# Performance work log

Hardware: AMD Instinct MI355X
Metric: run time of the kernel (lower is better)

Reference implementation:

```python
import jax, jax.numpy as jnp
import numpy as np
from jax.ops import segment_sum

N_NODES = 500000
N_EDGES = 1000000
N_GRAPHS = 20000
F_IN = 78


def gcn_conv(x, W, b, src, dst, n):
    # PyG GCNConv: add self-loops, symmetric normalization D^-1/2 A D^-1/2
    h = x @ W  # [N, Fout]
    deg = segment_sum(jnp.ones(src.shape[0], x.dtype), dst, num_segments=n) + 1.0  # self-loop
    dinv = jax.lax.rsqrt(deg)  # [N]
    norm = dinv[src] * dinv[dst]  # [E]
    agg = segment_sum(h[src] * norm[:, None], dst, num_segments=n)  # neighbor messages
    agg = agg + h * (dinv * dinv)[:, None]  # self-loop message
    return agg + b


def global_mean_pool(x, batch, n_graphs):
    s = segment_sum(x, batch, num_segments=n_graphs)
    cnt = segment_sum(jnp.ones(x.shape[0], x.dtype), batch, num_segments=n_graphs)
    return s / jnp.maximum(cnt, 1.0)[:, None]


def setup_inputs() -> dict:
    key = jax.random.key(0)
    ks = jax.random.split(key, 16)
    x = jax.random.normal(ks[0], (N_NODES, F_IN), dtype=jnp.float32)
    edge_index = jax.random.randint(ks[1], (2, N_EDGES), 0, N_NODES, dtype=jnp.int32)
    batch = jnp.sort(jax.random.randint(ks[2], (N_NODES,), 0, N_GRAPHS, dtype=jnp.int32))

    def lin(k, fi, fo):
        s = 1.0 / np.sqrt(fi)
        kw, kb = jax.random.split(k)
        return (jax.random.uniform(kw, (fi, fo), jnp.float32, -s, s),
                jax.random.uniform(kb, (fo,), jnp.float32, -s, s))

    W1, b1 = lin(ks[3], F_IN, F_IN)
    W2, b2 = lin(ks[4], F_IN, F_IN * 2)
    W3, b3 = lin(ks[5], F_IN * 2, F_IN * 4)
    fW1, fb1 = lin(ks[6], F_IN * 4, 1024)
    fW2, fb2 = lin(ks[7], 1024, 128)
    return {"x": x, "edge_index": edge_index, "batch": batch,
            "W1": W1, "b1": b1, "W2": W2, "b2": b2, "W3": W3, "b3": b3,
            "fW1": fW1, "fb1": fb1, "fW2": fW2, "fb2": fb2}


def reference(x, edge_index, batch, W1, b1, W2, b2, W3, b3, fW1, fb1, fW2, fb2):
    src, dst = edge_index[0], edge_index[1]
    n = x.shape[0]
    h = jax.nn.relu(gcn_conv(x, W1, b1, src, dst, n))
    h = jax.nn.relu(gcn_conv(h, W2, b2, src, dst, n))
    h = jax.nn.relu(gcn_conv(h, W3, b3, src, dst, n))
    g = global_mean_pool(h, batch, N_GRAPHS)  # [G, 312]
    g = jax.nn.relu(g @ fW1 + fb1)  # dropout is identity at eval
    return g @ fW2 + fb2
```

## Files before the change

kernel.cpp:

```cpp
#include <hip/hip_runtime.h>
#include <hip/hip_fp16.h>

#define N_NODES 500000
#define N_EDGES 1000000
#define N_GRAPHS 20000

typedef _Float16 f16x8 __attribute__((ext_vector_type(8)));
typedef float f32x4 __attribute__((ext_vector_type(4)));

__global__ __launch_bounds__(256) void fill_u32(unsigned* p, unsigned v, int n) {
  int i = blockIdx.x * 256 + threadIdx.x;
  if (i < n) p[i] = v;
}

__global__ __launch_bounds__(256) void hist_dst(const int* __restrict__ dst, int* cnt, int e) {
  int i = blockIdx.x * 256 + threadIdx.x;
  if (i < e) atomicAdd(&cnt[dst[i]], 1);
}

__global__ __launch_bounds__(256) void scanA(const int* __restrict__ deg, int* __restrict__ loc,
                                             int* __restrict__ partials, int n) {
  __shared__ int ts[256];
  int b = blockIdx.x, t = threadIdx.x;
  int base = b * 1024 + t * 4;
  int v[4], s = 0;
#pragma unroll
  for (int j = 0; j < 4; ++j) {
    v[j] = (base + j < n) ? deg[base + j] : 0;
    s += v[j];
  }
  ts[t] = s;
  __syncthreads();
  for (int off = 1; off < 256; off <<= 1) {
    int x = (t >= off) ? ts[t - off] : 0;
    __syncthreads();
    ts[t] += x;
    __syncthreads();
  }
  if (t == 255) partials[b] = ts[255];
  int run = ts[t] - s;
#pragma unroll
  for (int j = 0; j < 4; ++j) {
    if (base + j < n) loc[base + j] = run;
    run += v[j];
  }
}

__global__ __launch_bounds__(512) void scanB(int* partials, int nb) {
  __shared__ int s[512];
  int t = threadIdx.x;
  s[t] = (t < nb) ? partials[t] : 0;
  __syncthreads();
  if (t == 0) {
    int run = 0;
    for (int i = 0; i < nb; ++i) { int v = s[i]; s[i] = run; run += v; }
  }
  __syncthreads();
  if (t < nb) partials[t] = s[t];
}

__global__ __launch_bounds__(256) void scanC(int* __restrict__ rowptr, const int* __restrict__ partials,
                                             int* __restrict__ cur, int n, int e) {
  int i = blockIdx.x * 256 + threadIdx.x;
  if (i < n) {
    int v = rowptr[i] + partials[i >> 10];
    rowptr[i] = v;
    cur[i] = v;
  }
  if (i == 0) rowptr[n] = e;
}

__global__ __launch_bounds__(256) void dinv_k(const int* __restrict__ rowptr, float* dinv, int n) {
  int i = blockIdx.x * 256 + threadIdx.x;
  if (i < n) dinv[i] = rsqrtf(1.0f + (float)(rowptr[i + 1] - rowptr[i]));
}

__global__ __launch_bounds__(256) void bucket(const int* __restrict__ src, const int* __restrict__ dst,
                                              int* __restrict__ cur, int* __restrict__ ssrc, int e) {
  int i = blockIdx.x * 256 + threadIdx.x;
  if (i < e) ssrc[atomicAdd(&cur[dst[i]], 1)] = src[i];
}

__global__ __launch_bounds__(256) void ell_build(const int* __restrict__ rowptr,
                                                 const int* __restrict__ ssrc,
                                                 int4* __restrict__ ell, int n) {
  int i = blockIdx.x * 256 + threadIdx.x;
  if (i >= n) return;
  int r0 = rowptr[i], r1 = rowptr[i + 1];
  int deg = r1 - r0;
  int4 e;
  e.x = deg;
  e.y = (deg > 0) ? ssrc[r0] : 0;
  e.z = (deg > 1) ? ssrc[r0 + 1] : 0;
  e.w = (deg > 2) ? ssrc[r0 + 2] : 0;
  ell[i] = e;
}

__global__ __launch_bounds__(256) void graph_starts(const int* __restrict__ batch,
                                                    int* __restrict__ gstart, int n) {
  int i = blockIdx.x * 256 + threadIdx.x;
  if (i < n) {
    int b = batch[i];
    int bp = (i == 0) ? -1 : batch[i - 1];
    for (int g = bp + 1; g <= b; ++g) gstart[g] = i;
  } else if (i == n) {
    int bl = batch[n - 1];
    for (int g = bl + 1; g <= N_GRAPHS; ++g) gstart[g] = n;
  }
}

template <int CW>
__global__ __launch_bounds__(256) void wt_conv(const float* __restrict__ W, _Float16* __restrict__ WT,
                                               int K, int Nout, int ldw, int KPL, int STRIDE, int total) {
  int i = blockIdx.x * 256 + threadIdx.x;
  if (i >= total) return;
  int c = i / STRIDE, kp = i - c * STRIDE;
  int k = kp; bool valid = kp < KPL;
  if (CW) { int blk = kp / CW, r = kp - blk * CW; k = blk * 78 + r; valid = valid && (r < 78) && (k < K); }
  else { valid = valid && (kp < K); }
  WT[i] = (valid && c < Nout) ? (_Float16)W[(size_t)k * ldw + c] : (_Float16)0.f;
}

__global__ __launch_bounds__(256) void xconv(const float* __restrict__ xin,
                                             const float* __restrict__ dinv,
                                             _Float16* __restrict__ Xh) {
  unsigned idx = blockIdx.x * 256u + threadIdx.x;
  if (idx >= (unsigned)N_NODES * 52u) return;
  unsigned n = idx / 52u, c2 = idx - n * 52u;
  __half2 h = __floats2half2_rn(0.f, 0.f);
  if (c2 < 39u) {
    float di = dinv[n];
    float2 v = *reinterpret_cast<const float2*>(xin + (size_t)n * 78 + 2 * c2);
    h = __floats2half2_rn(v.x * di, v.y * di);
  }
  *reinterpret_cast<__half2*>((__half*)Xh + (size_t)n * 104 + 2 * c2) = h;
}

__device__ __forceinline__ void async16(const void* g, void* l) {
  __builtin_amdgcn_global_load_lds(
      (const __attribute__((address_space(1))) void*)g,
      (__attribute__((address_space(3))) void*)l, 16, 0, 0);
}

template <int KPL, int STRIDE, int OUT_MODE>
__global__ __launch_bounds__(256) void gemm_lds(
    const _Float16* __restrict__ in, const _Float16* __restrict__ WT,
    _Float16* __restrict__ outp, const float* __restrict__ rs,
    const float* __restrict__ bo, int M, int LDO) {
  constexpr int NS = KPL / 32;
  constexpr int SB = STRIDE * 2;
  constexpr int CA = (64 * SB) / 1024;
  constexpr int CB = (80 * SB + 1023) / 1024;
  __shared__ __align__(16) _Float16 As[64 * STRIDE];
  __shared__ __align__(16) _Float16 Bs[CB * 512];
  const int tid = threadIdx.x;
  const int lane = tid & 63;
  const int wid = tid >> 6;
  const int row0 = blockIdx.y * 64;
  const _Float16* wt = WT + (size_t)(blockIdx.x * 78) * STRIDE;
  _Float16* out = outp + (size_t)blockIdx.x * 80;
  const float* bop = bo + blockIdx.x * 78;

  const char* ab = (const char*)in + (size_t)row0 * SB;
  for (int c = wid; c < CA; c += 4)
    async16(ab + (size_t)c * 1024 + lane * 16, (char*)As + c * 1024);
  const char* bb = (const char*)wt;
  for (int c = wid; c < CB; c += 4)
    async16(bb + (size_t)c * 1024 + lane * 16, (char*)Bs + c * 1024);
  __syncthreads();

  const int r16 = lane & 15, q = lane >> 4;
  const f32x4 z4 = {0.f, 0.f, 0.f, 0.f};
  f32x4 acc[5];
#pragma unroll
  for (int nf = 0; nf < 5; ++nf) acc[nf] = z4;

#pragma unroll
  for (int s = 0; s < NS; ++s) {
    f16x8 af = *reinterpret_cast<const f16x8*>(&As[(wid * 16 + r16) * STRIDE + s * 32 + q * 8]);
#pragma unroll
    for (int nf = 0; nf < 5; ++nf) {
      f16x8 bf = *reinterpret_cast<const f16x8*>(&Bs[(nf * 16 + r16) * STRIDE + s * 32 + q * 8]);
      acc[nf] = __builtin_amdgcn_mfma_f32_16x16x32_f16(af, bf, acc[nf], 0, 0, 0);
    }
  }

  __syncthreads();
  _Float16* Os = As;
#pragma unroll
  for (int j = 0; j < 4; ++j) {
    int rl = wid * 16 + q * 4 + j;
    int gr = row0 + rl;
    float sc = (OUT_MODE == 3 && gr < M) ? rs[gr] : 1.f;
#pragma unroll
    for (int nf = 0; nf < 5; ++nf) {
      int cl = nf * 16 + r16;
      float v = 0.f;
      if (cl < 78) {
        v = fmaxf(acc[nf][j] + bop[cl], 0.f);
        if (OUT_MODE == 3) v *= sc;
      }
      Os[rl * 80 + cl] = (_Float16)v;
    }
  }
  __syncthreads();
  for (int i = tid; i < 640; i += 256) {
    int rl = i / 10, u = i - rl * 10;
    int gr = row0 + rl;
    if (gr < M)
      *reinterpret_cast<uint4*>(&out[(size_t)gr * LDO + u * 8]) =
          *reinterpret_cast<const uint4*>(&Os[rl * 80 + u * 8]);
  }
}

template <int KP, int OUT_MODE, int BLDS>
__global__ __launch_bounds__(256) void gemm_direct(
    const _Float16* __restrict__ in, const _Float16* __restrict__ WT,
    void* __restrict__ outp, const float* __restrict__ bo,
    int M, int Nout, int LDO) {
  constexpr int NS = KP / 32;
  constexpr bool TSTORE = (BLDS != 0) && (OUT_MODE != 2);
  constexpr int BS_BYTES = BLDS ? 5 * NS * 64 * 16 : 16;
  constexpr int SM_BYTES = TSTORE ? (BS_BYTES > 20480 ? BS_BYTES : 20480) : BS_BYTES;
  __shared__ __align__(16) char smem[SM_BYTES];
  _Float16* Bs = (_Float16*)smem;
  const int tid = threadIdx.x;
  const int lane = tid & 63;
  const int wid = tid >> 6;
  const int row0 = blockIdx.y * 128;
  const int col0 = blockIdx.x * 80;
  const _Float16* wt = WT + (size_t)col0 * KP;
  _Float16* out16 = (_Float16*)outp;
  float* out32 = (float*)outp;
  const int koff = (lane >> 4) * 8;
  const int gr0 = row0 + wid * 32 + (lane & 15);
  const bool v0 = gr0 < M, v1 = (gr0 + 16) < M;
  const _Float16* a0 = in + (size_t)gr0 * KP + koff;
  const _Float16* a1 = a0 + (size_t)16 * KP;
  const _Float16* bp = wt + (size_t)(lane & 15) * KP + koff;

  if (BLDS) {
    for (int i = tid; i < 5 * NS * 64; i += 256) {
      int l = i & 63;
      int nf = (i >> 6) % 5;
      int s = i / 320;
      int r = nf * 16 + (l & 15);
      int k = s * 32 + ((l >> 4) << 3);
      *reinterpret_cast<uint4*>(&Bs[(size_t)i * 8]) =
          *reinterpret_cast<const uint4*>(wt + (size_t)r * KP + k);
    }
    __syncthreads();
  }

  const f16x8 zf = {0, 0, 0, 0, 0, 0, 0, 0};
  const f32x4 z4 = {0.f, 0.f, 0.f, 0.f};
  f32x4 acc[2][5];
#pragma unroll
  for (int a = 0; a < 2; ++a)
#pragma unroll
    for (int b = 0; b < 5; ++b) acc[a][b] = z4;

#pragma unroll
  for (int s = 0; s < NS; ++s) {
    f16x8 af0 = v0 ? *reinterpret_cast<const f16x8*>(a0 + s * 32) : zf;
    f16x8 af1 = v1 ? *reinterpret_cast<const f16x8*>(a1 + s * 32) : zf;
    f16x8 bf[5];
#pragma unroll
    for (int nf = 0; nf < 5; ++nf) {
      if (BLDS)
        bf[nf] = *reinterpret_cast<const f16x8*>(&Bs[((size_t)(s * 5 + nf) * 64 + lane) * 8]);
      else
        bf[nf] = *reinterpret_cast<const f16x8*>(bp + (size_t)nf * 16 * KP + s * 32);
    }
#pragma unroll
    for (int nf = 0; nf < 5; ++nf) {
      acc[0][nf] = __builtin_amdgcn_mfma_f32_16x16x32_f16(af0, bf[nf], acc[0][nf], 0, 0, 0);
      acc[1][nf] = __builtin_amdgcn_mfma_f32_16x16x32_f16(af1, bf[nf], acc[1][nf], 0, 0, 0);
    }
  }

  if constexpr (TSTORE) {
    __syncthreads();
    _Float16* Os = (_Float16*)smem;
#pragma unroll
    for (int rf = 0; rf < 2; ++rf) {
#pragma unroll
      for (int j = 0; j < 4; ++j) {
        int rl = wid * 32 + rf * 16 + (lane >> 4) * 4 + j;
#pragma unroll
        for (int nf = 0; nf < 5; ++nf) {
          int cl = nf * 16 + (lane & 15);
          int oc = col0 + cl;
          float r = 0.f;
          if (oc < Nout) r = fmaxf(acc[rf][nf][j] + bo[oc], 0.f);
          Os[rl * 80 + cl] = (_Float16)r;
        }
      }
    }
    __syncthreads();
    for (int i = tid; i < 1280; i += 256) {
      int rl = i / 10, u = i - rl * 10;
      int gr = row0 + rl;
      if (gr < M)
        *reinterpret_cast<uint4*>(&out16[(size_t)gr * LDO + col0 + u * 8]) =
            *reinterpret_cast<const uint4*>(&Os[rl * 80 + u * 8]);
    }
  } else {
#pragma unroll
    for (int rf = 0; rf < 2; ++rf) {
#pragma unroll
      for (int j = 0; j < 4; ++j) {
        int gr = row0 + wid * 32 + rf * 16 + (lane >> 4) * 4 + j;
        if (gr >= M) continue;
#pragma unroll
        for (int nf = 0; nf < 5; ++nf) {
          int oc = col0 + nf * 16 + (lane & 15);
          if (oc >= Nout) continue;
          float v = acc[rf][nf][j];
          if (OUT_MODE == 1) out16[(size_t)gr * LDO + oc] = (_Float16)fmaxf(v + bo[oc], 0.f);
          else out32[(size_t)gr * LDO + oc] = v + bo[oc];
        }
      }
    }
  }
}

__device__ inline void acc8(float* a, uint4 v) {
  const __half2* h = reinterpret_cast<const __half2*>(&v);
#pragma unroll
  for (int j = 0; j < 4; ++j) {
    float2 f = __half22float2(h[j]);
    a[2 * j] += f.x;
    a[2 * j + 1] += f.y;
  }
}

template <int LDI>
__device__ inline void gather_sumT(float* a, const _Float16* hbase, unsigned n,
                                   const int4* __restrict__ ell,
                                   const int* __restrict__ rowptr,
                                   const int* __restrict__ ssrc) {
  int4 e = ell[n];
  const int deg = e.x;
  uint4 sv = *reinterpret_cast<const uint4*>(hbase + (size_t)n * LDI);
  uint4 g0, g1, g2;
  if (deg > 0) g0 = *reinterpret_cast<const uint4*>(hbase + (size_t)e.y * LDI);
  if (deg > 1) g1 = *reinterpret_cast<const uint4*>(hbase + (size_t)e.z * LDI);
  if (deg > 2) g2 = *reinterpret_cast<const uint4*>(hbase + (size_t)e.w * LDI);
  {
    const __half2* h = reinterpret_cast<const __half2*>(&sv);
#pragma unroll
    for (int j = 0; j < 4; ++j) {
      float2 f = __half22float2(h[j]);
      a[2 * j] = f.x;
      a[2 * j + 1] = f.y;
    }
  }
  if (deg > 0) acc8(a, g0);
  if (deg > 1) acc8(a, g1);
  if (deg > 2) acc8(a, g2);
  if (deg > 3) {
    int r = rowptr[n] + 3, r1 = r + deg - 3;
    for (; r + 2 <= r1; r += 2) {
      uint4 va = *reinterpret_cast<const uint4*>(hbase + (size_t)ssrc[r] * LDI);
      uint4 vb = *reinterpret_cast<const uint4*>(hbase + (size_t)ssrc[r + 1] * LDI);
      acc8(a, va);
      acc8(a, vb);
    }
    if (r < r1) {
      uint4 va = *reinterpret_cast<const uint4*>(hbase + (size_t)ssrc[r] * LDI);
      acc8(a, va);
    }
  }
}

template <int LDI, int NSUB>
__global__ __launch_bounds__(256) void aggregateZ(
    const _Float16* __restrict__ in, const int4* __restrict__ ell,
    const int* __restrict__ rowptr, const int* __restrict__ ssrc,
    const float* __restrict__ dinv, _Float16* __restrict__ outZ, int ldo) {
  unsigned idx = blockIdx.x * 256u + threadIdx.x;
  if (idx >= (unsigned)N_NODES * NSUB) return;
  unsigned n = idx / NSUB, sub = idx - n * NSUB;
  float a[8];
  gather_sumT<LDI>(a, in + sub * 8u, n, ell, rowptr, ssrc);
  float di = dinv[n];
  _Float16 ov[8];
#pragma unroll
  for (int j = 0; j < 8; ++j) ov[j] = (_Float16)(di * a[j]);
  *reinterpret_cast<uint4*>(outZ + (size_t)n * ldo + sub * 8u) =
      *reinterpret_cast<const uint4*>(ov);
}

__global__ __launch_bounds__(256) void pool_seq(
    const _Float16* __restrict__ in, const int* __restrict__ gstart,
    _Float16* __restrict__ GA, int inOff, int coffGA) {
  unsigned idx = blockIdx.x * 256u + threadIdx.x;
  if (idx >= (unsigned)N_GRAPHS * 10u) return;
  unsigned g = idx / 10u, q = idx - g * 10u;
  int n0 = gstart[g], n1 = gstart[g + 1];
  const _Float16* base = in + inOff + q * 8;
  float a[8] = {0.f, 0.f, 0.f, 0.f, 0.f, 0.f, 0.f, 0.f};
  float b2[8] = {0.f, 0.f, 0.f, 0.f, 0.f, 0.f, 0.f, 0.f};
  int n = n0;
  for (; n + 2 <= n1; n += 2) {
    uint4 va = *reinterpret_cast<const uint4*>(base + (size_t)n * 168);
    uint4 vb = *reinterpret_cast<const uint4*>(base + (size_t)(n + 1) * 168);
    acc8(a, va);
    acc8(b2, vb);
  }
  if (n < n1) {
    uint4 va = *reinterpret_cast<const uint4*>(base + (size_t)n * 168);
    acc8(a, va);
  }
  float gi = 1.0f / fmaxf((float)(n1 - n0), 1.0f);
  _Float16 ov[8];
#pragma unroll
  for (int j = 0; j < 8; ++j) ov[j] = (_Float16)((a[j] + b2[j]) * gi);
  *reinterpret_cast<uint4*>(GA + (size_t)g * 320 + coffGA + q * 8) =
      *reinterpret_cast<const uint4*>(ov);
}

extern "C" void kernel_launch(void* const* d_in, const int* in_sizes, int n_in,
                              void* d_out, int out_size, void* d_ws, size_t ws_size,
                              hipStream_t stream) {
  const float* x   = (const float*)d_in[0];
  const int* ei    = (const int*)d_in[1];
  const int* batch = (const int*)d_in[2];
  const float* W1 = (const float*)d_in[3];
  const float* b1 = (const float*)d_in[4];
  const float* W2 = (const float*)d_in[5];
  const float* b2 = (const float*)d_in[6];
  const float* W3 = (const float*)d_in[7];
  const float* b3 = (const float*)d_in[8];
  const float* fW1 = (const float*)d_in[9];
  const float* fb1 = (const float*)d_in[10];
  const float* fW2 = (const float*)d_in[11];
  const float* fb2 = (const float*)d_in[12];
  float* out = (float*)d_out;

  const int Nn = N_NODES, E = N_EDGES, G = N_GRAPHS;
  const int* src = ei;
  const int* dst = ei + E;

  _Float16* A = (_Float16*)d_ws;
  _Float16* B = A + (size_t)Nn * 168;
  _Float16* GA = B + (size_t)Nn * 168;
  _Float16* W1T   = GA + (size_t)G * 320;
  _Float16* W2T   = W1T + 96 * 104;
  _Float16* W3T   = W2T + 160 * 104;
  _Float16* fW1T  = W3T + 320 * 168;
  _Float16* fW2T  = fW1T + (size_t)1040 * 320;
  float* dinv     = (float*)(fW2T + (size_t)160 * 1056);
  int* rowptr     = (int*)(dinv + Nn);
  int* cur        = rowptr + Nn + 1;
  int* ssrc       = cur + Nn;
  int* partials   = ssrc + E;
  int* gstart     = partials + 512;
  int4* ell = (int4*)(((uintptr_t)(gstart + G + 1) + 15) & ~(uintptr_t)15);

  _Float16* Xh = A;
  _Float16* Z1 = B;
  _Float16* H1 = A;
  _Float16* Z2 = B;
  _Float16* H2 = A;
  _Float16* Z3 = B;
  _Float16* O3 = A;
  _Float16* fc1 = B;

  dim3 blk(256);
  const int gN13 = (int)(((unsigned)Nn * 13u + 255u) / 256u);
  const int gN20 = (int)(((unsigned)Nn * 20u + 255u) / 256u);
  const int gG10 = (int)(((unsigned)G * 10u + 255u) / 256u);
  const dim3 oneGrid(1, (Nn + 63) / 64);
  const dim3 pairGrid(2, (Nn + 63) / 64);
  const int NB = (Nn + 1023) / 1024;

  fill_u32<<<(Nn + 255) / 256, blk, 0, stream>>>((unsigned*)cur, 0u, Nn);
  hist_dst<<<(E + 255) / 256, blk, 0, stream>>>(dst, cur, E);
  scanA<<<NB, blk, 0, stream>>>(cur, rowptr, partials, Nn);
  scanB<<<1, 512, 0, stream>>>(partials, NB);
  scanC<<<(Nn + 255) / 256, blk, 0, stream>>>(rowptr, partials, cur, Nn, E);
  dinv_k<<<(Nn + 255) / 256, blk, 0, stream>>>(rowptr, dinv, Nn);
  bucket<<<(E + 255) / 256, blk, 0, stream>>>(src, dst, cur, ssrc, E);
  ell_build<<<(Nn + 255) / 256, blk, 0, stream>>>(rowptr, ssrc, ell, Nn);
  graph_starts<<<(Nn + 256) / 256, blk, 0, stream>>>(batch, gstart, Nn);

  wt_conv<0><<<(96 * 104 + 255) / 256, blk, 0, stream>>>(W1, W1T, 78, 78, 78, 96, 104, 96 * 104);
  wt_conv<0><<<(160 * 104 + 255) / 256, blk, 0, stream>>>(W2, W2T, 78, 156, 156, 96, 104, 160 * 104);
  wt_conv<80><<<(320 * 168 + 255) / 256, blk, 0, stream>>>(W3, W3T, 156, 312, 312, 160, 168, 320 * 168);
  wt_conv<80><<<(1040 * 320 + 255) / 256, blk, 0, stream>>>(fW1, fW1T, 312, 1024, 1024, 320, 320, 1040 * 320);
  wt_conv<0><<<(160 * 1056 + 255) / 256, blk, 0, stream>>>(fW2, fW2T, 1024, 128, 128, 1056, 1056, 160 * 1056);

  xconv<<<(int)(((unsigned)Nn * 52u + 255u) / 256u), blk, 0, stream>>>(x, dinv, Xh);

  aggregateZ<104, 13><<<gN13, blk, 0, stream>>>(Xh, ell, rowptr, ssrc, dinv, Z1, 104);
  gemm_lds<96, 104, 3><<<oneGrid, blk, 0, stream>>>(Z1, W1T, H1, dinv, b1, Nn, 104);

  aggregateZ<104, 13><<<gN13, blk, 0, stream>>>(H1, ell, rowptr, ssrc, dinv, Z2, 104);
  gemm_lds<96, 104, 3><<<pairGrid, blk, 0, stream>>>(Z2, W2T, H2, dinv, b2, Nn, 168);

  aggregateZ<168, 20><<<gN20, blk, 0, stream>>>(H2, ell, rowptr, ssrc, dinv, Z3, 168);
  for (int p = 0; p < 2; ++p) {
    gemm_lds<160, 168, 1><<<pairGrid, blk, 0, stream>>>(
        Z3, W3T + (size_t)(156 * p) * 168, O3, nullptr, b3 + 156 * p, Nn, 168);
    pool_seq<<<gG10, blk, 0, stream>>>(O3, gstart, GA, 0, (2 * p) * 80);
    pool_seq<<<gG10, blk, 0, stream>>>(O3, gstart, GA, 80, (2 * p + 1) * 80);
  }

  {
    dim3 g((1024 + 79) / 80, (G + 127) / 128);
    gemm_direct<320, 1, 1><<<g, blk, 0, stream>>>(GA, fW1T, fc1, fb1, G, 1024, 1056);
  }
  {
    dim3 g((128 + 79) / 80, (G + 127) / 128);
    gemm_direct<1056, 2, 0><<<g, blk, 0, stream>>>(fc1, fW2T, out, fb2, G, 128, 128);
  }
}
```

Before: 1.030 ms.

## Fuse global mean pooling into layer-3 GEMM epilogue via segmented atomics

The layer-3 GEMM now covers all four 78-column output chunks in one launch and, in its epilogue, sums the post-ReLU rows per graph ID (using sorted batch) and atomically adds the partial sums into a float accumulator. The full 500k x 312 intermediate is no longer written to memory and the four pool_seq passes that read it back are gone. A small scale kernel divides by node counts and converts to fp16, and a fill kernel zeroes the accumulator. The cost is float atomics, a serial 64-row loop run by only 78 threads per block, and a non-deterministic summation order.

Measured after the change: 1.158 ms. 1.12x slower.

```diff
diff --git a/kernel.cpp b/kernel.cpp
--- a/kernel.cpp
+++ b/kernel.cpp
@@ -142,23 +142,24 @@
       (__attribute__((address_space(3))) void*)l, 16, 0, 0);
 }
 
-template <int KPL, int STRIDE, int OUT_MODE>
+template <int KPL, int STRIDE, int OUT_MODE, int POOL>
 __global__ __launch_bounds__(256) void gemm_lds(
     const _Float16* __restrict__ in, const _Float16* __restrict__ WT,
     _Float16* __restrict__ outp, const float* __restrict__ rs,
-    const float* __restrict__ bo, int M, int LDO) {
+    const float* __restrict__ bo, int M, int LDO,
+    const int* __restrict__ batch, float* __restrict__ gsum) {
   constexpr int NS = KPL / 32;
   constexpr int SB = STRIDE * 2;
   constexpr int CA = (64 * SB) / 1024;
   constexpr int CB = (80 * SB + 1023) / 1024;
   __shared__ __align__(16) _Float16 As[64 * STRIDE];
   __shared__ __align__(16) _Float16 Bs[CB * 512];
+  __shared__ int sBatch[POOL ? 64 : 1];
   const int tid = threadIdx.x;
   const int lane = tid & 63;
   const int wid = tid >> 6;
   const int row0 = blockIdx.y * 64;
   const _Float16* wt = WT + (size_t)(blockIdx.x * 78) * STRIDE;
-  _Float16* out = outp + (size_t)blockIdx.x * 80;
   const float* bop = bo + blockIdx.x * 78;
 
   const char* ab = (const char*)in + (size_t)row0 * SB;
@@ -203,13 +204,38 @@
       Os[rl * 80 + cl] = (_Float16)v;
     }
   }
+  if (POOL && tid < 64) {
+    int gr = row0 + tid;
+    sBatch[tid] = (gr < M) ? batch[gr] : -1;
+  }
   __syncthreads();
-  for (int i = tid; i < 640; i += 256) {
-    int rl = i / 10, u = i - rl * 10;
-    int gr = row0 + rl;
-    if (gr < M)
-      *reinterpret_cast<uint4*>(&out[(size_t)gr * LDO + u * 8]) =
-          *reinterpret_cast<const uint4*>(&Os[rl * 80 + u * 8]);
+
+  if constexpr (POOL) {
+    if (tid < 78) {
+      const int gcol = blockIdx.x * 80 + tid;
+      float sum = 0.f;
+      int gcur = -2;
+      for (int r = 0; r < 64; ++r) {
+        int g = sBatch[r];
+        if (g < 0) break;
+        if (g != gcur) {
+          if (gcur >= 0) atomicAdd(&gsum[(size_t)gcur * 320 + gcol], sum);
+          gcur = g;
+          sum = 0.f;
+        }
+        sum += (float)Os[r * 80 + tid];
+      }
+      if (gcur >= 0) atomicAdd(&gsum[(size_t)gcur * 320 + gcol], sum);
+    }
+  } else {
+    _Float16* out = outp + (size_t)blockIdx.x * 80;
+    for (int i = tid; i < 640; i += 256) {
+      int rl = i / 10, u = i - rl * 10;
+      int gr = row0 + rl;
+      if (gr < M)
+        *reinterpret_cast<uint4*>(&out[(size_t)gr * LDO + u * 8]) =
+            *reinterpret_cast<const uint4*>(&Os[rl * 80 + u * 8]);
+    }
   }
 }
 
@@ -392,33 +418,14 @@
       *reinterpret_cast<const uint4*>(ov);
 }
 
-__global__ __launch_bounds__(256) void pool_seq(
-    const _Float16* __restrict__ in, const int* __restrict__ gstart,
-    _Float16* __restrict__ GA, int inOff, int coffGA) {
-  unsigned idx = blockIdx.x * 256u + threadIdx.x;
-  if (idx >= (unsigned)N_GRAPHS * 10u) return;
-  unsigned g = idx / 10u, q = idx - g * 10u;
-  int n0 = gstart[g], n1 = gstart[g + 1];
-  const _Float16* base = in + inOff + q * 8;
-  float a[8] = {0.f, 0.f, 0.f, 0.f, 0.f, 0.f, 0.f, 0.f};
-  float b2[8] = {0.f, 0.f, 0.f, 0.f, 0.f, 0.f, 0.f, 0.f};
-  int n = n0;
-  for (; n + 2 <= n1; n += 2) {
-    uint4 va = *reinterpret_cast<const uint4*>(base + (size_t)n * 168);
-    uint4 vb = *reinterpret_cast<const uint4*>(base + (size_t)(n + 1) * 168);
-    acc8(a, va);
-    acc8(b2, vb);
-  }
-  if (n < n1) {
-    uint4 va = *reinterpret_cast<const uint4*>(base + (size_t)n * 168);
-    acc8(a, va);
-  }
-  float gi = 1.0f / fmaxf((float)(n1 - n0), 1.0f);
-  _Float16 ov[8];
-#pragma unroll
-  for (int j = 0; j < 8; ++j) ov[j] = (_Float16)((a[j] + b2[j]) * gi);
-  *reinterpret_cast<uint4*>(GA + (size_t)g * 320 + coffGA + q * 8) =
-      *reinterpret_cast<const uint4*>(ov);
+__global__ __launch_bounds__(256) void ga_scale(
+    const float* __restrict__ gsum, const int* __restrict__ gstart,
+    _Float16* __restrict__ GA) {
+  int i = blockIdx.x * 256 + threadIdx.x;
+  if (i >= N_GRAPHS * 320) return;
+  int g = i / 320;
+  float gi = 1.0f / fmaxf((float)(gstart[g + 1] - gstart[g]), 1.0f);
+  GA[i] = (_Float16)(gsum[i] * gi);
 }
 
 extern "C" void kernel_launch(void* const* d_in, const int* in_sizes, int n_in,
@@ -446,7 +453,8 @@
   _Float16* A = (_Float16*)d_ws;
   _Float16* B = A + (size_t)Nn * 168;
   _Float16* GA = B + (size_t)Nn * 168;
-  _Float16* W1T   = GA + (size_t)G * 320;
+  float*    gsum = (float*)(GA + (size_t)G * 320);
+  _Float16* W1T   = (_Float16*)(gsum + (size_t)G * 320);
   _Float16* W2T   = W1T + 96 * 104;
   _Float16* W3T   = W2T + 160 * 104;
   _Float16* fW1T  = W3T + 320 * 168;
@@ -465,15 +473,14 @@
   _Float16* Z2 = B;
   _Float16* H2 = A;
   _Float16* Z3 = B;
-  _Float16* O3 = A;
-  _Float16* fc1 = B;
+  _Float16* fc1 = A;
 
   dim3 blk(256);
   const int gN13 = (int)(((unsigned)Nn * 13u + 255u) / 256u);
   const int gN20 = (int)(((unsigned)Nn * 20u + 255u) / 256u);
-  const int gG10 = (int)(((unsigned)G * 10u + 255u) / 256u);
   const dim3 oneGrid(1, (Nn + 63) / 64);
   const dim3 pairGrid(2, (Nn + 63) / 64);
+  const dim3 quadGrid(4, (Nn + 63) / 64);
   const int NB = (Nn + 1023) / 1024;
 
   fill_u32<<<(Nn + 255) / 256, blk, 0, stream>>>((unsigned*)cur, 0u, Nn);
@@ -492,21 +499,19 @@
   wt_conv<80><<<(1040 * 320 + 255) / 256, blk, 0, stream>>>(fW1, fW1T, 312, 1024, 1024, 320, 320, 1040 * 320);
   wt_conv<0><<<(160 * 1056 + 255) / 256, blk, 0, stream>>>(fW2, fW2T, 1024, 128, 128, 1056, 1056, 160 * 1056);
 
+  fill_u32<<<(G * 320 + 255) / 256, blk, 0, stream>>>((unsigned*)gsum, 0u, G * 320);
   xconv<<<(int)(((unsigned)Nn * 52u + 255u) / 256u), blk, 0, stream>>>(x, dinv, Xh);
 
   aggregateZ<104, 13><<<gN13, blk, 0, stream>>>(Xh, ell, rowptr, ssrc, dinv, Z1, 104);
-  gemm_lds<96, 104, 3><<<oneGrid, blk, 0, stream>>>(Z1, W1T, H1, dinv, b1, Nn, 104);
+  gemm_lds<96, 104, 3, 0><<<oneGrid, blk, 0, stream>>>(Z1, W1T, H1, dinv, b1, Nn, 104, nullptr, nullptr);
 
   aggregateZ<104, 13><<<gN13, blk, 0, stream>>>(H1, ell, rowptr, ssrc, dinv, Z2, 104);
-  gemm_lds<96, 104, 3><<<pairGrid, blk, 0, stream>>>(Z2, W2T, H2, dinv, b2, Nn, 168);
+  gemm_lds<96, 104, 3, 0><<<pairGrid, blk, 0, stream>>>(Z2, W2T, H2, dinv, b2, Nn, 168, nullptr, nullptr);
 
   aggregateZ<168, 20><<<gN20, blk, 0, stream>>>(H2, ell, rowptr, ssrc, dinv, Z3, 168);
-  for (int p = 0; p < 2; ++p) {
-    gemm_lds<160, 168, 1><<<pairGrid, blk, 0, stream>>>(
-        Z3, W3T + (size_t)(156 * p) * 168, O3, nullptr, b3 + 156 * p, Nn, 168);
-    pool_seq<<<gG10, blk, 0, stream>>>(O3, gstart, GA, 0, (2 * p) * 80);
-    pool_seq<<<gG10, blk, 0, stream>>>(O3, gstart, GA, 80, (2 * p + 1) * 80);
-  }
+  gemm_lds<160, 168, 1, 1><<<quadGrid, blk, 0, stream>>>(Z3, W3T, nullptr, nullptr, b3, Nn, 0, batch, gsum);
+
+  ga_scale<<<(G * 320 + 255) / 256, blk, 0, stream>>>(gsum, gstart, GA);
 
   {
     dim3 g((1024 + 79) / 80, (G + 127) / 128);
```
